# Kernel tuning notes

Measured on AMD Instinct MI355X. Metric: run time of the kernel, lower is better.

The kernel has to match this reference:

```python
import jax, jax.numpy as jnp
import numpy as np

B, S, HID, NH, HD, NL = 2, 4096, 1024, 16, 64, 128
N_ITER = 6


def setup_inputs() -> dict:
    key = jax.random.key(0)
    ks = jax.random.split(key, 9)
    s = 0.02
    D = NH * HD
    return {
        "X": jax.random.normal(ks[0], (B, S, HID), jnp.float32),
        "mask": jnp.ones((B, S), jnp.float32),
        "Wq": jax.random.normal(ks[1], (HID, D), jnp.float32) * s,
        "bq": jnp.zeros((D,), jnp.float32),
        "Wk": jax.random.normal(ks[2], (HID, D), jnp.float32) * s,
        "bk": jnp.zeros((D,), jnp.float32),
        "Wv": jax.random.normal(ks[3], (HID, D), jnp.float32) * s,
        "bv": jnp.zeros((D,), jnp.float32),
        "Wo": jax.random.normal(ks[4], (D, HID), jnp.float32) * s,
        "bo": jnp.zeros((HID,), jnp.float32),
    }


def iterative_inv(mat, n_iter=N_ITER):
    # Newton-Schulz style pseudo-inverse iteration (Nystromformer 'original' init)
    I = jnp.eye(mat.shape[-1], dtype=mat.dtype)
    K = mat
    V = K.swapaxes(-1, -2) / jnp.max(jnp.sum(K, axis=-2))
    for _ in range(n_iter):
        KV = K @ V
        V = 0.25 * V @ (13.0 * I - KV @ (15.0 * I - KV @ (7.0 * I - KV)))
    return V


def nystrom_core(Q, K, V, mask):
    # Q,K,V: [B,NH,S,HD], mask: [B,S]
    scale = 1.0 / np.sqrt(np.sqrt(HD))  # 1/d^(1/4) applied to both Q and K
    m = mask[:, None, :, None]
    Q = Q * m * scale
    K = K * m * scale
    seg = S // NL
    # landmarks: mean over contiguous segments -> [B,NH,NL,HD]
    Ql = Q.reshape(B, NH, NL, seg, HD).mean(axis=-2)
    Kl = K.reshape(B, NH, NL, seg, HD).mean(axis=-2)
    k1 = jax.nn.softmax(jnp.einsum('bhsd,bhld->bhsl', Q, Kl), axis=-1)   # [B,NH,S,NL]
    k2 = jax.nn.softmax(jnp.einsum('bhld,bhmd->bhlm', Ql, Kl), axis=-1)  # [B,NH,NL,NL]
    k3 = jax.nn.softmax(
        jnp.einsum('bhld,bhsd->bhls', Ql, K) - 1e9 * (1.0 - mask[:, None, None, :]),
        axis=-1)                                                          # [B,NH,NL,S]
    return k1 @ iterative_inv(k2) @ (k3 @ V)                              # [B,NH,S,HD]


def reference(X, mask, Wq, bq, Wk, bk, Wv, bv, Wo, bo):
    def split(Y):  # [B,S,NH*HD] -> [B,NH,S,HD]
        return Y.reshape(B, S, NH, HD).transpose(0, 2, 1, 3)
    Q = split(X @ Wq + bq)
    K = split(X @ Wk + bk)
    V = split(X @ Wv + bv)
    attn = nystrom_core(Q.astype(jnp.float32), K.astype(jnp.float32),
                        V.astype(jnp.float32), mask.astype(jnp.float32))
    out = attn.transpose(0, 2, 1, 3).reshape(B, S, NH * HD)
    return out @ Wo + bo
```

## Files before the change

### kernel.cpp

```cpp
#include <hip/hip_runtime.h>
#include <math.h>

constexpr int cB = 2, cS = 4096, cHID = 1024, cNH = 16, cHD = 64, cNL = 128, cSEG = 32, cD = 1024, cBH = 32;
constexpr float cSCALE = 0.35355339059327373f;

typedef _Float16 f16x8 __attribute__((ext_vector_type(8)));
typedef float f32x4 __attribute__((ext_vector_type(4)));

__device__ inline void gload_lds16(const void* g, void* l) {
    __builtin_amdgcn_global_load_lds(
        (const __attribute__((address_space(1))) void*)g,
        (__attribute__((address_space(3))) void*)l, 16, 0, 0);
}

__global__ __launch_bounds__(256) void wcast_t(
    const float* __restrict__ Wq, const float* __restrict__ Wk,
    const float* __restrict__ Wv, const float* __restrict__ Wo,
    _Float16* __restrict__ WqT, _Float16* __restrict__ WkT,
    _Float16* __restrict__ WvT, _Float16* __restrict__ WoT)
{
    __shared__ float tile[32][33];
    const int wsel = blockIdx.z;
    const float* W = (wsel == 0) ? Wq : (wsel == 1 ? Wk : (wsel == 2 ? Wv : Wo));
    _Float16* WT   = (wsel == 0) ? WqT : (wsel == 1 ? WkT : (wsel == 2 ? WvT : WoT));
    const int n0 = blockIdx.x * 32, k0 = blockIdx.y * 32;
    const int t = threadIdx.x;
    const int r = t >> 3, c = (t & 7) * 4;
    float4 v = *reinterpret_cast<const float4*>(W + (size_t)(k0 + r) * cD + n0 + c);
    tile[r][c] = v.x; tile[r][c + 1] = v.y; tile[r][c + 2] = v.z; tile[r][c + 3] = v.w;
    __syncthreads();
    union { _Float16 h[4]; ushort4 u; } p;
    p.h[0] = (_Float16)tile[c + 0][r]; p.h[1] = (_Float16)tile[c + 1][r];
    p.h[2] = (_Float16)tile[c + 2][r]; p.h[3] = (_Float16)tile[c + 3][r];
    *reinterpret_cast<ushort4*>(WT + (size_t)(n0 + r) * cHID + k0 + c) = p.u;
}

__global__ __launch_bounds__(256) void xm_kernel(
    const float* __restrict__ X, const float* __restrict__ mask,
    float* __restrict__ Xm, float* __restrict__ mbar, _Float16* __restrict__ Xh)
{
    const int bl = blockIdx.x;
    const int b = bl >> 7, l = bl & 127;
    const int c = threadIdx.x * 4;
    float4 a = {0.f, 0.f, 0.f, 0.f};
    float msum = 0.f;
    for (int j = 0; j < cSEG; ++j) {
        float m = mask[b * cS + l * cSEG + j];
        size_t roff = ((size_t)(b * cS + l * cSEG + j)) * cHID + c;
        float4 x = *reinterpret_cast<const float4*>(X + roff);
        union { _Float16 h[4]; ushort4 u; } p;
        p.h[0] = (_Float16)x.x; p.h[1] = (_Float16)x.y;
        p.h[2] = (_Float16)x.z; p.h[3] = (_Float16)x.w;
        *reinterpret_cast<ushort4*>(Xh + roff) = p.u;
        a.x += m * x.x; a.y += m * x.y; a.z += m * x.z; a.w += m * x.w;
        msum += m;
    }
    const float inv = 1.0f / cSEG;
    a.x *= inv; a.y *= inv; a.z *= inv; a.w *= inv;
    *reinterpret_cast<float4*>(Xm + (size_t)bl * cHID + c) = a;
    if (threadIdx.x == 0) mbar[bl] = msum * inv;
}

__global__ __launch_bounds__(256) void qkv_gemm_f16(
    const _Float16* __restrict__ Xh, const float* __restrict__ mask,
    const _Float16* __restrict__ WqT, const _Float16* __restrict__ WkT, const _Float16* __restrict__ WvT,
    const float* __restrict__ bq, const float* __restrict__ bk, const float* __restrict__ bv,
    _Float16* __restrict__ Qh, _Float16* __restrict__ Kh, _Float16* __restrict__ Vh)
{
    __shared__ __align__(16) _Float16 As[128 * 64];
    __shared__ __align__(16) _Float16 Bs[128 * 64];
    const int wsel = blockIdx.z;
    const _Float16* WT = (wsel == 0) ? WqT : (wsel == 1 ? WkT : WvT);
    const float* bias  = (wsel == 0) ? bq  : (wsel == 1 ? bk  : bv);
    _Float16* Y        = (wsel == 0) ? Qh  : (wsel == 1 ? Kh  : Vh);
    const int orig = blockIdx.x;
    const int xcd = orig & 7, idx = orig >> 3;
    const int n0 = (idx & 7) * 128;
    const int m0 = (xcd * 8 + (idx >> 3)) * 128;
    const int t = threadIdx.x;
    const int wave = t >> 6, lane = t & 63;
    const int wm = (wave >> 1) * 64, wn = (wave & 1) * 64;
    const int quad = lane >> 4, l15 = lane & 15;
    const int srow = wave * 8 + (lane >> 3);
    const int scol = ((lane & 7) ^ (lane >> 3)) * 8;

    f32x4 acc[4][4];
#pragma unroll
    for (int i = 0; i < 4; ++i)
#pragma unroll
        for (int j = 0; j < 4; ++j) acc[i][j] = (f32x4){0.f, 0.f, 0.f, 0.f};

    for (int k0 = 0; k0 < cHID; k0 += 64) {
        const _Float16* aSrc = Xh + (size_t)(m0 + srow) * cHID + k0 + scol;
// ... 180 lines not shown
#pragma unroll
    for (int u = 0; u < 16; ++u) {
        float4 a = q4[u], b = kl4[u];
        dot += a.x * b.x + a.y * b.y + a.z * b.z + a.w * b.w;
    }
    red[j] = dot; __syncthreads();
    for (int off = 64; off > 0; off >>= 1) { if (j < off) red[j] = fmaxf(red[j], red[j + off]); __syncthreads(); }
    float m = red[0]; __syncthreads();
    float e = expf(dot - m);
    red[j] = e; __syncthreads();
    for (int off = 64; off > 0; off >>= 1) { if (j < off) red[j] += red[j + off]; __syncthreads(); }
    k2[(bh * cNL + i) * cNL + j] = e / red[0];
}

__global__ __launch_bounds__(128) void colsum_max(const float* __restrict__ k2, int* __restrict__ cmax)
{
    __shared__ float red[128];
    int bh = blockIdx.x, j = threadIdx.x;
    float s = 0.f;
    for (int i = 0; i < cNL; ++i) s += k2[(bh * cNL + i) * cNL + j];
    red[j] = s; __syncthreads();
    for (int off = 64; off > 0; off >>= 1) { if (j < off) red[j] = fmaxf(red[j], red[j + off]); __syncthreads(); }
    if (j == 0) atomicMax(cmax, __float_as_int(red[0]));
}

__device__ inline void split2(float v, _Float16& h, _Float16& l) {
    h = (_Float16)v;
    l = (_Float16)(v - (float)h);
}
__device__ inline unsigned short f16bits(_Float16 h) { return __builtin_bit_cast(unsigned short, h); }

#define NYS_MFMA(a, b, c) __builtin_amdgcn_mfma_f32_16x16x32_f16((a), (b), (c), 0, 0, 0)

#define NYS_PRELOAD(PH, PL, LH, LL)                                                     \
    {                                                                                   \
        _Pragma("unroll")                                                               \
        for (int mt_ = 0; mt_ < 4; ++mt_) {                                             \
            const int rowL_ = wr * 64 + mt_ * 16 + l15;                                 \
            _Pragma("unroll")                                                           \
            for (int k0_ = 0; k0_ < 4; ++k0_) {                                         \
                LH[mt_][k0_] = *reinterpret_cast<const f16x8*>(&PH[rowL_ * 136 + k0_ * 32 + quad * 8]); \
                LL[mt_][k0_] = *reinterpret_cast<const f16x8*>(&PL[rowL_ * 136 + k0_ * 32 + quad * 8]); \
            }                                                                           \
        }                                                                               \
    }

#define NYS_PRODUCT(PH, PL, LH, LL)                                                     \
    {                                                                                   \
        _Pragma("unroll")                                                               \
        for (int mt_ = 0; mt_ < 4; ++mt_)                                               \
            _Pragma("unroll")                                                           \
            for (int nt_ = 0; nt_ < 2; ++nt_) acc[mt_][nt_] = (f32x4){0.f, 0.f, 0.f, 0.f}; \
        _Pragma("unroll")                                                               \
        for (int nt_ = 0; nt_ < 2; ++nt_) {                                             \
            _Pragma("unroll")                                                           \
            for (int k0_ = 0; k0_ < 4; ++k0_) {                                         \
                const int boff_ = (wcb + nt_ * 16) * 136 + k0_ * 32 + quad * 8;         \
                f16x8 bh_ = *reinterpret_cast<const f16x8*>(&PH[boff_]);                \
                f16x8 bl_ = *reinterpret_cast<const f16x8*>(&PL[boff_]);                \
                _Pragma("unroll")                                                       \
                for (int mt_ = 0; mt_ < 4; ++mt_) {                                     \
                    acc[mt_][nt_] = NYS_MFMA(LH[mt_][k0_], bh_, acc[mt_][nt_]);         \
                    acc[mt_][nt_] = NYS_MFMA(LL[mt_][k0_], bh_, acc[mt_][nt_]);         \
                    acc[mt_][nt_] = NYS_MFMA(LH[mt_][k0_], bl_, acc[mt_][nt_]);         \
                }                                                                       \
            }                                                                           \
        }                                                                               \
    }

__global__ __launch_bounds__(512, 2) void nys_fused(
    const float* __restrict__ k2, const int* __restrict__ cmax,
    float* __restrict__ Mg0, float* __restrict__ Mg1)
{
    __shared__ __align__(16) _Float16 Ahi_s[128 * 136];
    __shared__ __align__(16) _Float16 Alo_s[128 * 136];
    __shared__ __align__(16) _Float16 Whi_s[128 * 136];
    __shared__ __align__(16) _Float16 Wlo_s[128 * 136];
    const int bh = blockIdx.x;
    const int t = threadIdx.x;
    const int wave = t >> 6, lane = t & 63;
    const int wr = wave >> 2, wc = wave & 3;
    const int quad = lane >> 4, l15 = lane & 15;
    const int wcb = wc * 32 + l15;
    const float* Kg = k2 + (size_t)bh * 16384;
    float* Mg0b = Mg0 + (size_t)bh * 16384;
    float* Mg1b = Mg1 + (size_t)bh * 16384;
    const float sc = sqrtf(1.0f / __int_as_float(*cmax));

    {
        const int row = t >> 2, c0 = (t & 3) * 32;
        const float* src = Kg + row * 128 + c0;
        _Float16* dh = &Whi_s[row * 136 + c0];
        _Float16* dl = &Wlo_s[row * 136 + c0];
#pragma unroll
        for (int u = 0; u < 32; u += 4) {
            float4 v = *reinterpret_cast<const float4*>(src + u);
            ushort4 ph, pl; _Float16 h, l;
            split2(v.x * sc, h, l); ph.x = f16bits(h); pl.x = f16bits(l);
            split2(v.y * sc, h, l); ph.y = f16bits(h); pl.y = f16bits(l);
            split2(v.z * sc, h, l); ph.z = f16bits(h); pl.z = f16bits(l);
            split2(v.w * sc, h, l); ph.w = f16bits(h); pl.w = f16bits(l);
            *reinterpret_cast<ushort4*>(dh + u) = ph;
            *reinterpret_cast<ushort4*>(dl + u) = pl;
        }
    }
    __syncthreads();

    f32x4 acc[4][2];
    f16x8 Fh[4][4], Fl[4][4];

    NYS_PRELOAD(Whi_s, Wlo_s, Fh, Fl);
    NYS_PRODUCT(Whi_s, Wlo_s, Fh, Fl);
#pragma unroll
    for (int mt = 0; mt < 4; ++mt)
#pragma unroll
        for (int nt = 0; nt < 2; ++nt) {
            const int col = wcb + nt * 16;
            const int rb  = wr * 64 + mt * 16 + quad * 4;
            ushort4 ph, pl;
#pragma unroll
            for (int r = 0; r < 4; ++r) {
                _Float16 h, l; split2(acc[mt][nt][r], h, l);
                ((unsigned short*)&ph)[r] = f16bits(h);
                ((unsigned short*)&pl)[r] = f16bits(l);
            }
            *reinterpret_cast<ushort4*>(&Ahi_s[col * 136 + rb]) = ph;
            *reinterpret_cast<ushort4*>(&Alo_s[col * 136 + rb]) = pl;
        }
    __syncthreads();

    for (int it = 0; it < 6; ++it) {
        NYS_PRELOAD(Ahi_s, Alo_s, Fh, Fl);
        NYS_PRODUCT(Ahi_s, Alo_s, Fh, Fl);
#pragma unroll
        for (int mt = 0; mt < 4; ++mt)
#pragma unroll
            for (int nt = 0; nt < 2; ++nt) {
                const int col = wcb + nt * 16;
                const int rb  = wr * 64 + mt * 16 + quad * 4;
                ushort4 ah = *reinterpret_cast<const ushort4*>(&Ahi_s[col * 136 + rb]);
                ushort4 al = *reinterpret_cast<const ushort4*>(&Alo_s[col * 136 + rb]);
                ushort4 ph, pl;
#pragma unroll
                for (int r = 0; r < 4; ++r) {
                    float av = (float)__builtin_bit_cast(_Float16, ((unsigned short*)&ah)[r])
                             + (float)__builtin_bit_cast(_Float16, ((unsigned short*)&al)[r]);
                    float v = ((rb + r) == col ? 15.0f : 0.0f) - 7.0f * av + acc[mt][nt][r];
                    _Float16 h, l; split2(v, h, l);
                    ((unsigned short*)&ph)[r] = f16bits(h);
                    ((unsigned short*)&pl)[r] = f16bits(l);
                }
                *reinterpret_cast<ushort4*>(&Whi_s[col * 136 + rb]) = ph;
                *reinterpret_cast<ushort4*>(&Wlo_s[col * 136 + rb]) = pl;
            }
        __syncthreads();
        NYS_PRODUCT(Whi_s, Wlo_s, Fh, Fl);
        __syncthreads();
#pragma unroll
        for (int mt = 0; mt < 4; ++mt)
#pragma unroll
            for (int nt = 0; nt < 2; ++nt) {
                const int col = wcb + nt * 16;
                const int rb  = wr * 64 + mt * 16 + quad * 4;
                ushort4 ph, pl; float4 mv;
#pragma unroll
                for (int r = 0; r < 4; ++r) {
                    float v = ((rb + r) == col ? 13.0f : 0.0f) - acc[mt][nt][r];
                    _Float16 h, l; split2(v, h, l);
                    ((unsigned short*)&ph)[r] = f16bits(h);
                    ((unsigned short*)&pl)[r] = f16bits(l);
                    ((float*)&mv)[r] = 0.25f * v;
                }
                *reinterpret_cast<ushort4*>(&Whi_s[col * 136 + rb]) = ph;
                *reinterpret_cast<ushort4*>(&Wlo_s[col * 136 + rb]) = pl;
                if (it == 0)
                    *reinterpret_cast<float4*>(&Mg0b[col * 128 + rb]) = mv;
            }
        __syncthreads();
        NYS_PRODUCT(Whi_s, Wlo_s, Fh, Fl);
#pragma unroll
        for (int mt = 0; mt < 4; ++mt)
#pragma unroll
            for (int nt = 0; nt < 2; ++nt) {
                const int col = wcb + nt * 16;
                const int rb  = wr * 64 + mt * 16 + quad * 4;
                ushort4 ph, pl;
#pragma unroll
                for (int r = 0; r < 4; ++r) {
                    _Float16 h, l; split2(0.25f * acc[mt][nt][r], h, l);
                    ((unsigned short*)&ph)[r] = f16bits(h);
                    ((unsigned short*)&pl)[r] = f16bits(l);
                }
                *reinterpret_cast<ushort4*>(&Ahi_s[col * 136 + rb]) = ph;
                *reinterpret_cast<ushort4*>(&Alo_s[col * 136 + rb]) = pl;
            }
        if (it >= 1) {
            const float* Mr = (it & 1) ? Mg0b : Mg1b;
            float*       Mw = (it & 1) ? Mg1b : Mg0b;
#pragma unroll
            for (int mt = 0; mt < 4; ++mt)
#pragma unroll
                for (int nt = 0; nt < 2; ++nt) acc[mt][nt] = (f32x4){0.f, 0.f, 0.f, 0.f};
#pragma unroll
            for (int k0 = 0; k0 < 4; ++k0) {
                f16x8 Mh[4], Ml[4];
#pragma unroll
                for (int mt = 0; mt < 4; ++mt) {
                    const int rowL = wr * 64 + mt * 16 + l15;
                    const float* src = Mr + rowL * 128 + k0 * 32 + quad * 8;
                    float4 v0 = *reinterpret_cast<const float4*>(src);
                    float4 v1 = *reinterpret_cast<const float4*>(src + 4);
                    union { f16x8 v; _Float16 e[8]; } hh, ll;
                    split2(v0.x, hh.e[0], ll.e[0]); split2(v0.y, hh.e[1], ll.e[1]);
                    split2(v0.z, hh.e[2], ll.e[2]); split2(v0.w, hh.e[3], ll.e[3]);
                    split2(v1.x, hh.e[4], ll.e[4]); split2(v1.y, hh.e[5], ll.e[5]);
                    split2(v1.z, hh.e[6], ll.e[6]); split2(v1.w, hh.e[7], ll.e[7]);
                    Mh[mt] = hh.v; Ml[mt] = ll.v;
                }
#pragma unroll
                for (int nt = 0; nt < 2; ++nt) {
                    const int boff = (wcb + nt * 16) * 136 + k0 * 32 + quad * 8;
                    f16x8 bh_ = *reinterpret_cast<const f16x8*>(&Whi_s[boff]);
                    f16x8 bl_ = *reinterpret_cast<const f16x8*>(&Wlo_s[boff]);
#pragma unroll
                    for (int mt = 0; mt < 4; ++mt) {
                        acc[mt][nt] = NYS_MFMA(Mh[mt], bh_, acc[mt][nt]);
                        acc[mt][nt] = NYS_MFMA(Ml[mt], bh_, acc[mt][nt]);
                        acc[mt][nt] = NYS_MFMA(Mh[mt], bl_, acc[mt][nt]);
                    }
                }
            }
#pragma unroll
            for (int mt = 0; mt < 4; ++mt)
#pragma unroll
                for (int nt = 0; nt < 2; ++nt) {
                    const int col = wcb + nt * 16;
                    const int rb  = wr * 64 + mt * 16 + quad * 4;
                    float4 mv;
#pragma unroll
                    for (int r = 0; r < 4; ++r) ((float*)&mv)[r] = 0.25f * acc[mt][nt][r];
                    *reinterpret_cast<float4*>(&Mw[col * 128 + rb]) = mv;
                }
        }
        __syncthreads();
    }
}

__global__ __launch_bounds__(256) void vtrans(const _Float16* __restrict__ Vh, _Float16* __restrict__ VTh)
{
    __shared__ ushort T[64][72];
    const int s0 = blockIdx.x * 64, bh = blockIdx.y;
    const int t = threadIdx.x;
    const _Float16* vb = Vh + ((size_t)bh * cS + s0) * cHD;
#pragma unroll
    for (int i = 0; i < 2; ++i) {
        int idx = t + i * 256;
        int row = idx >> 3, c8 = idx & 7;
        f16x8 v = *reinterpret_cast<const f16x8*>(vb + (size_t)row * cHD + c8 * 8);
#pragma unroll
        for (int j = 0; j < 8; ++j) T[row][c8 * 8 + j] = ((ushort*)&v)[j];
    }
    __syncthreads();
    _Float16* vt = VTh + (size_t)bh * cHD * cS;
#pragma unroll
    for (int i = 0; i < 2; ++i) {
        int idx = t + i * 256;
        int d = idx >> 3, s8 = idx & 7;
        f16x8 o;
#pragma unroll
        for (int j = 0; j < 8; ++j) ((ushort*)&o)[j] = T[s8 * 8 + j][d];
        *reinterpret_cast<f16x8*>(vt + (size_t)d * cS + s0 + s8 * 8) = o;
    }
}

__global__ __launch_bounds__(256) void k3v_mfma(
    const _Float16* __restrict__ Qlh, const _Float16* __restrict__ Kh,
    const _Float16* __restrict__ VTh, const float* __restrict__ mask,
    float* __restrict__ Opart, float* __restrict__ mpart, float* __restrict__ spart)
{
    __shared__ __align__(16) _Float16 Ps[128 * 72];
    __shared__ float msk[256];
    const int z = blockIdx.x, bh = blockIdx.y;
    const int b = bh >> 4;
    const int sbase = z * 256;
    const int t = threadIdx.x;
    const int wave = t >> 6, lane = t & 63;
    const int quad = lane >> 4, l15 = lane & 15;

    msk[t] = mask[b * cS + sbase + t];

    f16x8 aq[2][2];
    const _Float16* qlg = Qlh + (size_t)bh * cNL * cHD;
#pragma unroll
    for (int mt = 0; mt < 2; ++mt)
#pragma unroll
        for (int k0 = 0; k0 < 2; ++k0)
            aq[mt][k0] = *reinterpret_cast<const f16x8*>(
                qlg + (size_t)(wave * 32 + mt * 16 + l15) * cHD + k0 * 32 + quad * 8);

    float mrun[2][4], srun[2][4];
    f32x4 accO[2][4];
#pragma unroll
    for (int mt = 0; mt < 2; ++mt)
#pragma unroll
        for (int r = 0; r < 4; ++r) { mrun[mt][r] = -1e30f; srun[mt][r] = 0.f; }
#pragma unroll
    for (int mt = 0; mt < 2; ++mt)
#pragma unroll
        for (int dt = 0; dt < 4; ++dt) accO[mt][dt] = (f32x4){0.f, 0.f, 0.f, 0.f};

    __syncthreads();

    const _Float16* kg = Kh + (size_t)bh * cS * cHD;
    const _Float16* vg = VTh + (size_t)bh * cHD * cS;

    for (int step = 0; step < 4; ++step) {
        const int st = sbase + step * 64;
        f32x4 accS[2][4];
#pragma unroll
        for (int mt = 0; mt < 2; ++mt)
#pragma unroll
            for (int nt = 0; nt < 4; ++nt) accS[mt][nt] = (f32x4){0.f, 0.f, 0.f, 0.f};
#pragma unroll
        for (int k0 = 0; k0 < 2; ++k0)
#pragma unroll
            for (int nt = 0; nt < 4; ++nt) {
                f16x8 bk = *reinterpret_cast<const f16x8*>(
                    kg + (size_t)(st + nt * 16 + l15) * cHD + k0 * 32 + quad * 8);
#pragma unroll
                for (int mt = 0; mt < 2; ++mt)
                    accS[mt][nt] = __builtin_amdgcn_mfma_f32_16x16x32_f16(aq[mt][k0], bk, accS[mt][nt], 0, 0, 0);
            }
#pragma unroll
        for (int nt = 0; nt < 4; ++nt) {
            float pen = 1e9f * (1.0f - msk[step * 64 + nt * 16 + l15]);
#pragma unroll
            for (int mt = 0; mt < 2; ++mt)
#pragma unroll
                for (int r = 0; r < 4; ++r) accS[mt][nt][r] -= pen;
        }
#pragma unroll
        for (int mt = 0; mt < 2; ++mt) {
#pragma unroll
            for (int r = 0; r < 4; ++r) {
                float tmax = fmaxf(fmaxf(accS[mt][0][r], accS[mt][1][r]),
                                   fmaxf(accS[mt][2][r], accS[mt][3][r]));
#pragma unroll
                for (int w = 1; w < 16; w <<= 1) tmax = fmaxf(tmax, __shfl_xor(tmax, w, 16));
                float mnew = fmaxf(mrun[mt][r], tmax);
                float alpha = __expf(mrun[mt][r] - mnew);
                float ts = 0.f;
#pragma unroll
                for (int nt = 0; nt < 4; ++nt) {
                    float e = __expf(accS[mt][nt][r] - mnew);
                    accS[mt][nt][r] = e; ts += e;
                }
#pragma unroll
                for (int w = 1; w < 16; w <<= 1) ts += __shfl_xor(ts, w, 16);
                srun[mt][r] = srun[mt][r] * alpha + ts;
                mrun[mt][r] = mnew;
#pragma unroll
                for (int dt = 0; dt < 4; ++dt) accO[mt][dt][r] *= alpha;
            }
        }
#pragma unroll
        for (int mt = 0; mt < 2; ++mt)
#pragma unroll
            for (int nt = 0; nt < 4; ++nt)
#pragma unroll
                for (int r = 0; r < 4; ++r)
                    Ps[(wave * 32 + mt * 16 + quad * 4 + r) * 72 + nt * 16 + l15] =
                        (_Float16)accS[mt][nt][r];
#pragma unroll
        for (int k0 = 0; k0 < 2; ++k0) {
            f16x8 ap[2];
#pragma unroll
            for (int mt = 0; mt < 2; ++mt)
                ap[mt] = *reinterpret_cast<const f16x8*>(
                    &Ps[(wave * 32 + mt * 16 + l15) * 72 + k0 * 32 + quad * 8]);
#pragma unroll
            for (int dt = 0; dt < 4; ++dt) {
                f16x8 bv = *reinterpret_cast<const f16x8*>(
                    vg + (size_t)(dt * 16 + l15) * cS + st + k0 * 32 + quad * 8);
#pragma unroll
                for (int mt = 0; mt < 2; ++mt)
                    accO[mt][dt] = __builtin_amdgcn_mfma_f32_16x16x32_f16(ap[mt], bv, accO[mt][dt], 0, 0, 0);
            }
        }
    }
    const int rowbase = bh * cNL + wave * 32;
#pragma unroll
    for (int mt = 0; mt < 2; ++mt)
#pragma unroll
        for (int dt = 0; dt < 4; ++dt)
#pragma unroll
            for (int r = 0; r < 4; ++r)
                Opart[(size_t)(z * 4096 + rowbase + mt * 16 + quad * 4 + r) * cHD + dt * 16 + l15] =
                    accO[mt][dt][r];
    if (l15 == 0) {
#pragma unroll
        for (int mt = 0; mt < 2; ++mt)
#pragma unroll
            for (int r = 0; r < 4; ++r) {
                int prow = z * 4096 + rowbase + mt * 16 + quad * 4 + r;
                mpart[prow] = mrun[mt][r];
                spart[prow] = srun[mt][r];
            }
    }
}

__global__ __launch_bounds__(256) void k3v_reduce(
    const float* __restrict__ Opart, const float* __restrict__ mpart,
    const float* __restrict__ spart, float* __restrict__ CV)
{
    const int t = threadIdx.x;
    const int row = blockIdx.x * 4 + (t >> 6);
    const int d = t & 63;
    float mstar = -1e30f;
#pragma unroll
    for (int z = 0; z < 16; ++z) mstar = fmaxf(mstar, mpart[z * 4096 + row]);
    float ssum = 0.f, acc = 0.f;
#pragma unroll
    for (int z = 0; z < 16; ++z) {
        float w = __expf(mpart[z * 4096 + row] - mstar);
        ssum += w * spart[z * 4096 + row];
        acc  += w * Opart[(size_t)(z * 4096 + row) * cHD + d];
    }
    CV[(size_t)row * cHD + d] = acc / ssum;
}

__global__ __launch_bounds__(256) void w2_matmul(
    const float* __restrict__ k2, const float* __restrict__ M6,
    const int* __restrict__ cmax, const float* __restrict__ CV,
    _Float16* __restrict__ W2T)
{
    __shared__ __align__(16) float CVs[128][68];
    __shared__ __align__(16) float Us[128][68];
    const int bh = blockIdx.x, t = threadIdx.x;
    const float invc = 1.0f / __int_as_float(*cmax);
    for (int k = 0; k < 32; ++k) { int idx = t + k * 256; CVs[idx >> 6][idx & 63] = CV[(size_t)bh * 8192 + idx]; }
// ... 129 lines not shown
{
    const float* X    = (const float*)d_in[0];
    const float* mask = (const float*)d_in[1];
    const float* Wq   = (const float*)d_in[2];
    const float* bq   = (const float*)d_in[3];
    const float* Wk   = (const float*)d_in[4];
    const float* bk   = (const float*)d_in[5];
    const float* Wv   = (const float*)d_in[6];
    const float* bv   = (const float*)d_in[7];
    const float* Wo   = (const float*)d_in[8];
    const float* bo   = (const float*)d_in[9];
    float* out = (float*)d_out;

    float* ws = (float*)d_ws;
    size_t off = 0;
    const size_t szQKV = (size_t)cBH * cS * cHD;
    const size_t szL   = (size_t)cBH * cNL * cHD;
    const size_t szM   = (size_t)cBH * cNL * cNL;
    float* Qr   = ws + off; off += szQKV;
    float* Kr   = ws + off; off += szQKV;
    float* Vr   = ws + off; off += szQKV;
    _Float16* Xh  = (_Float16*)(ws + off); off += szQKV / 2;
    _Float16* WqT = (_Float16*)(ws + off); off += 524288;
    _Float16* WkT = (_Float16*)(ws + off); off += 524288;
    _Float16* WvT = (_Float16*)(ws + off); off += 524288;
    _Float16* WoT = (_Float16*)(ws + off); off += 524288;
    float* Xm   = ws + off; off += (size_t)cB * cNL * cHID;
    float* mbar = ws + off; off += 256;
    float* Ql  = ws + off; off += szL;
    float* Kl  = ws + off; off += szL;
    float* k2  = ws + off; off += szM;
    float* Mg0 = ws + off; off += szM;
    float* Mg1 = ws + off; off += szM;
    float* Zb  = ws + off; off += szM;
    float* T2b = ws + off; off += szM;
    float* T3b = ws + off; off += szM;
    float* CV  = ws + off; off += szL;
    _Float16* Qlh  = (_Float16*)(ws + off); off += szL / 2;
    _Float16* Klh  = (_Float16*)(ws + off); off += szL / 2;
    _Float16* W2Th = (_Float16*)(ws + off); off += szL / 2;
    int*   cmax = (int*)(ws + off); off += 16;
    float* mpart = ws + off; off += 65536;
    float* spart = ws + off; off += 65536;

    _Float16* Qh   = (_Float16*)Qr;
    float*    Opart = Qr + szQKV / 2;
    _Float16* Kh   = (_Float16*)Kr;
    _Float16* ctxh = (_Float16*)(Kr + szQKV / 2);
    _Float16* Vh   = (_Float16*)Vr;
    _Float16* VTh  = (_Float16*)(Vr + szQKV / 2);

    (void)Zb; (void)T2b; (void)T3b;

    hipMemsetAsync(cmax, 0, sizeof(int), stream);

    wcast_t<<<dim3(32, 32, 4), 256, 0, stream>>>(Wq, Wk, Wv, Wo, WqT, WkT, WvT, WoT);
    xm_kernel<<<cB * cNL, 256, 0, stream>>>(X, mask, Xm, mbar, Xh);

    qkv_gemm_f16<<<dim3(512, 1, 3), 256, 0, stream>>>(
        Xh, mask, WqT, WkT, WvT, bq, bk, bv, Qh, Kh, Vh);
    vtrans<<<dim3(cS / 64, cBH), 256, 0, stream>>>(Vh, VTh);
    lgemm<<<dim3(cD / 64, (cB * cNL) / 64, 2), 256, 0, stream>>>(Xm, mbar, Wq, bq, Wk, bk, Ql, Kl, Qlh, Klh);

    k2_softmax<<<cBH * cNL, 128, 0, stream>>>(Ql, Kl, k2);
    colsum_max<<<cBH, 128, 0, stream>>>(k2, cmax);

    nys_fused<<<cBH, 512, 0, stream>>>(k2, cmax, Mg0, Mg1);

    k3v_mfma<<<dim3(16, cBH), 256, 0, stream>>>(Qlh, Kh, VTh, mask, Opart, mpart, spart);
    k3v_reduce<<<1024, 256, 0, stream>>>(Opart, mpart, spart, CV);
    w2_matmul<<<cBH, 256, 0, stream>>>(k2, Mg1, cmax, CV, W2Th);
    k1_mfma<<<dim3(cS / 64, cBH), 256, 0, stream>>>(Qh, Klh, W2Th, ctxh);
    out_gemm_f16<<<dim3(512), 256, 0, stream>>>(ctxh, WoT, bo, out);
}
```

Baseline: 474.2 us.

## Fuse Nystrom inverse and k3V into one launch and halve inverse-kernel LDS

The Newton-Schulz inverse kernel (32 blocks) and the k3·V flash-style kernel (16×32 blocks) are merged into one launch keyed on blockIdx. The independent k3V work now runs alongside the long serial inverse iterations instead of after them. To fit two blocks per CU with the k3V blocks, the inverse path keeps only the W operand in LDS and reads the A matrix from a global fp32 scratch buffer, splitting it to hi/lo fp16 on the fly. This adds global traffic and conversion work inside the iteration. The xm_kernel is also reshaped to use 4× more blocks of 64 threads for more parallelism.

```diff
diff --git a/kernel.cpp b/kernel.cpp
--- a/kernel.cpp
+++ b/kernel.cpp
@@ -35,13 +35,14 @@
     *reinterpret_cast<ushort4*>(WT + (size_t)(n0 + r) * cHID + k0 + c) = p.u;
 }
 
-__global__ __launch_bounds__(256) void xm_kernel(
+__global__ __launch_bounds__(64) void xm_kernel(
     const float* __restrict__ X, const float* __restrict__ mask,
     float* __restrict__ Xm, float* __restrict__ mbar, _Float16* __restrict__ Xh)
 {
     const int bl = blockIdx.x;
+    const int q  = blockIdx.y;
     const int b = bl >> 7, l = bl & 127;
-    const int c = threadIdx.x * 4;
+    const int c = q * 256 + threadIdx.x * 4;
     float4 a = {0.f, 0.f, 0.f, 0.f};
     float msum = 0.f;
     for (int j = 0; j < cSEG; ++j) {
@@ -58,7 +59,7 @@
     const float inv = 1.0f / cSEG;
     a.x *= inv; a.y *= inv; a.z *= inv; a.w *= inv;
     *reinterpret_cast<float4*>(Xm + (size_t)bl * cHID + c) = a;
-    if (threadIdx.x == 0) mbar[bl] = msum * inv;
+    if (q == 0 && threadIdx.x == 0) mbar[bl] = msum * inv;
 }
 
 __global__ __launch_bounds__(256) void qkv_gemm_f16(
@@ -305,7 +306,7 @@
 
 #define NYS_MFMA(a, b, c) __builtin_amdgcn_mfma_f32_16x16x32_f16((a), (b), (c), 0, 0, 0)
 
-#define NYS_PRELOAD(PH, PL, LH, LL)                                                     \
+#define NYS_PRELOAD_LDS(PH, PL, LH, LL)                                                 \
     {                                                                                   \
         _Pragma("unroll")                                                               \
         for (int mt_ = 0; mt_ < 4; ++mt_) {                                             \
@@ -318,7 +319,27 @@
         }                                                                               \
     }
 
-#define NYS_PRODUCT(PH, PL, LH, LL)                                                     \
+#define NYS_PRELOAD_G(GP, LH, LL)                                                       \
+    {                                                                                   \
+        _Pragma("unroll")                                                               \
+        for (int mt_ = 0; mt_ < 4; ++mt_) {                                             \
+            const int rowL_ = wr * 64 + mt_ * 16 + l15;                                 \
+            _Pragma("unroll")                                                           \
+            for (int k0_ = 0; k0_ < 4; ++k0_) {                                         \
+                const float* s_ = GP + rowL_ * 128 + k0_ * 32 + quad * 8;               \
+                float4 v0_ = *reinterpret_cast<const float4*>(s_);                      \
+                float4 v1_ = *reinterpret_cast<const float4*>(s_ + 4);                  \
+                union { f16x8 v; _Float16 e[8]; } hh_, ll_;                             \
+                split2(v0_.x, hh_.e[0], ll_.e[0]); split2(v0_.y, hh_.e[1], ll_.e[1]);   \
+                split2(v0_.z, hh_.e[2], ll_.e[2]); split2(v0_.w, hh_.e[3], ll_.e[3]);   \
+                split2(v1_.x, hh_.e[4], ll_.e[4]); split2(v1_.y, hh_.e[5], ll_.e[5]);   \
+                split2(v1_.z, hh_.e[6], ll_.e[6]); split2(v1_.w, hh_.e[7], ll_.e[7]);   \
+                LH[mt_][k0_] = hh_.v; LL[mt_][k0_] = ll_.v;                             \
+            }                                                                           \
+        }                                                                               \
+    }
+
+#define NYS_PRODUCT_LDS(PH, PL, LH, LL)                                                 \
     {                                                                                   \
         _Pragma("unroll")                                                               \
         for (int mt_ = 0; mt_ < 4; ++mt_)                                               \
@@ -341,168 +362,141 @@
         }                                                                               \
     }
 
-__global__ __launch_bounds__(512, 2) void nys_fused(
+#define NYS_PRODUCT_G(GP, LH, LL)                                                       \
+    {                                                                                   \
+        _Pragma("unroll")                                                               \
+        for (int mt_ = 0; mt_ < 4; ++mt_)                                               \
+            _Pragma("unroll")                                                           \
+            for (int nt_ = 0; nt_ < 2; ++nt_) acc[mt_][nt_] = (f32x4){0.f, 0.f, 0.f, 0.f}; \
+        _Pragma("unroll")                                                               \
+        for (int nt_ = 0; nt_ < 2; ++nt_) {                                             \
+            _Pragma("unroll")                                                           \
+            for (int k0_ = 0; k0_ < 4; ++k0_) {                                         \
+                const float* s_ = GP + (wcb + nt_ * 16) * 128 + k0_ * 32 + quad * 8;    \
+                float4 v0_ = *reinterpret_cast<const float4*>(s_);                      \
+                float4 v1_ = *reinterpret_cast<const float4*>(s_ + 4);                  \
+                union { f16x8 v; _Float16 e[8]; } bh_, bl_;                             \
+                split2(v0_.x, bh_.e[0], bl_.e[0]); split2(v0_.y, bh_.e[1], bl_.e[1]);   \
+                split2(v0_.z, bh_.e[2], bl_.e[2]); split2(v0_.w, bh_.e[3], bl_.e[3]);   \
+                split2(v1_.x, bh_.e[4], bl_.e[4]); split2(v1_.y, bh_.e[5], bl_.e[5]);   \
+                split2(v1_.z, bh_.e[6], bl_.e[6]); split2(v1_.w, bh_.e[7], bl_.e[7]);   \
+                _Pragma("unroll")                                                       \
+                for (int mt_ = 0; mt_ < 4; ++mt_) {                                     \
+                    acc[mt_][nt_] = NYS_MFMA(LH[mt_][k0_], bh_.v, acc[mt_][nt_]);       \
+                    acc[mt_][nt_] = NYS_MFMA(LL[mt_][k0_], bh_.v, acc[mt_][nt_]);       \
+                    acc[mt_][nt_] = NYS_MFMA(LH[mt_][k0_], bl_.v, acc[mt_][nt_]);       \
+                }                                                                       \
+            }                                                                           \
+        }                                                                               \
+    }
+
+__global__ __launch_bounds__(512, 2) void nys_k3v(
     const float* __restrict__ k2, const int* __restrict__ cmax,
-    float* __restrict__ Mg0, float* __restrict__ Mg1)
-{
-    __shared__ __align__(16) _Float16 Ahi_s[128 * 136];
-    __shared__ __align__(16) _Float16 Alo_s[128 * 136];
-    __shared__ __align__(16) _Float16 Whi_s[128 * 136];
-    __shared__ __align__(16) _Float16 Wlo_s[128 * 136];
-    const int bh = blockIdx.x;
-    const int t = threadIdx.x;
-    const int wave = t >> 6, lane = t & 63;
-    const int wr = wave >> 2, wc = wave & 3;
-    const int quad = lane >> 4, l15 = lane & 15;
-    const int wcb = wc * 32 + l15;
-    const float* Kg = k2 + (size_t)bh * 16384;
-    float* Mg0b = Mg0 + (size_t)bh * 16384;
-    float* Mg1b = Mg1 + (size_t)bh * 16384;
-    const float sc = sqrtf(1.0f / __int_as_float(*cmax));
-
-    {
-        const int row = t >> 2, c0 = (t & 3) * 32;
-        const float* src = Kg + row * 128 + c0;
-        _Float16* dh = &Whi_s[row * 136 + c0];
-        _Float16* dl = &Wlo_s[row * 136 + c0];
-#pragma unroll
-        for (int u = 0; u < 32; u += 4) {
-            float4 v = *reinterpret_cast<const float4*>(src + u);
-            ushort4 ph, pl; _Float16 h, l;
-            split2(v.x * sc, h, l); ph.x = f16bits(h); pl.x = f16bits(l);
-            split2(v.y * sc, h, l); ph.y = f16bits(h); pl.y = f16bits(l);
-            split2(v.z * sc, h, l); ph.z = f16bits(h); pl.z = f16bits(l);
-            split2(v.w * sc, h, l); ph.w = f16bits(h); pl.w = f16bits(l);
-            *reinterpret_cast<ushort4*>(dh + u) = ph;
-            *reinterpret_cast<ushort4*>(dl + u) = pl;
-        }
-    }
-    __syncthreads();
-
-    f32x4 acc[4][2];
-    f16x8 Fh[4][4], Fl[4][4];
-
-    NYS_PRELOAD(Whi_s, Wlo_s, Fh, Fl);
-    NYS_PRODUCT(Whi_s, Wlo_s, Fh, Fl);
-#pragma unroll
-    for (int mt = 0; mt < 4; ++mt)
-#pragma unroll
-        for (int nt = 0; nt < 2; ++nt) {
-            const int col = wcb + nt * 16;
-            const int rb  = wr * 64 + mt * 16 + quad * 4;
-            ushort4 ph, pl;
-#pragma unroll
-            for (int r = 0; r < 4; ++r) {
-                _Float16 h, l; split2(acc[mt][nt][r], h, l);
-                ((unsigned short*)&ph)[r] = f16bits(h);
-                ((unsigned short*)&pl)[r] = f16bits(l);
+    float* __restrict__ Ag_all, float* __restrict__ Mg0, float* __restrict__ Mg1,
+    const _Float16* __restrict__ Qlh, const _Float16* __restrict__ Kh,
+    const _Float16* __restrict__ VTh, const float* __restrict__ mask,
+    float* __restrict__ Opart, float* __restrict__ mpart, float* __restrict__ spart)
+{
+    __shared__ __align__(16) _Float16 SMEM[2 * 128 * 136];
+
+    if (blockIdx.x < 32) {
+        _Float16* Wh = SMEM;
+        _Float16* Wl = SMEM + 128 * 136;
+        const int bh = blockIdx.x;
+        const int t = threadIdx.x;
+        const int wave = t >> 6, lane = t & 63;
+        const int wr = wave >> 2, wc = wave & 3;
+        const int quad = lane >> 4, l15 = lane & 15;
+        const int wcb = wc * 32 + l15;
+        const float* Kg = k2 + (size_t)bh * 16384;
+        float* Ag   = Ag_all + (size_t)bh * 16384;
+        float* Mg0b = Mg0 + (size_t)bh * 16384;
+        float* Mg1b = Mg1 + (size_t)bh * 16384;
+        const float sc = sqrtf(1.0f / __int_as_float(*cmax));
+
+        {
+            const int row = t >> 2, c0 = (t & 3) * 32;
+            const float* src = Kg + row * 128 + c0;
+            _Float16* dh = &Wh[row * 136 + c0];
+            _Float16* dl = &Wl[row * 136 + c0];
+#pragma unroll
+            for (int u = 0; u < 32; u += 4) {
+                float4 v = *reinterpret_cast<const float4*>(src + u);
+                ushort4 ph, pl; _Float16 h, l;
+                split2(v.x * sc, h, l); ph.x = f16bits(h); pl.x = f16bits(l);
+                split2(v.y * sc, h, l); ph.y = f16bits(h); pl.y = f16bits(l);
+                split2(v.z * sc, h, l); ph.z = f16bits(h); pl.z = f16bits(l);
+                split2(v.w * sc, h, l); ph.w = f16bits(h); pl.w = f16bits(l);
+                *reinterpret_cast<ushort4*>(dh + u) = ph;
+                *reinterpret_cast<ushort4*>(dl + u) = pl;
             }
-            *reinterpret_cast<ushort4*>(&Ahi_s[col * 136 + rb]) = ph;
-            *reinterpret_cast<ushort4*>(&Alo_s[col * 136 + rb]) = pl;
-        }
-    __syncthreads();
-
-    for (int it = 0; it < 6; ++it) {
-        NYS_PRELOAD(Ahi_s, Alo_s, Fh, Fl);
-        NYS_PRODUCT(Ahi_s, Alo_s, Fh, Fl);
+        }
+        __syncthreads();
+
+        f32x4 acc[4][2];
+        f16x8 Fh[4][4], Fl[4][4];
+
+        NYS_PRELOAD_LDS(Wh, Wl, Fh, Fl);
+        NYS_PRODUCT_LDS(Wh, Wl, Fh, Fl);
 #pragma unroll
         for (int mt = 0; mt < 4; ++mt)
 #pragma unroll
             for (int nt = 0; nt < 2; ++nt) {
                 const int col = wcb + nt * 16;
                 const int rb  = wr * 64 + mt * 16 + quad * 4;
-                ushort4 ah = *reinterpret_cast<const ushort4*>(&Ahi_s[col * 136 + rb]);
-                ushort4 al = *reinterpret_cast<const ushort4*>(&Alo_s[col * 136 + rb]);
-                ushort4 ph, pl;
-#pragma unroll
-                for (int r = 0; r < 4; ++r) {
-                    float av = (float)__builtin_bit_cast(_Float16, ((unsigned short*)&ah)[r])
-                             + (float)__builtin_bit_cast(_Float16, ((unsigned short*)&al)[r]);
-                    float v = ((rb + r) == col ? 15.0f : 0.0f) - 7.0f * av + acc[mt][nt][r];
-                    _Float16 h, l; split2(v, h, l);
-                    ((unsigned short*)&ph)[r] = f16bits(h);
-                    ((unsigned short*)&pl)[r] = f16bits(l);
-                }
-                *reinterpret_cast<ushort4*>(&Whi_s[col * 136 + rb]) = ph;
-                *reinterpret_cast<ushort4*>(&Wlo_s[col * 136 + rb]) = pl;
+                float4 mv;
+#pragma unroll
+                for (int r = 0; r < 4; ++r) ((float*)&mv)[r] = acc[mt][nt][r];
+                *reinterpret_cast<float4*>(&Ag[col * 128 + rb]) = mv;
             }
         __syncthreads();
-        NYS_PRODUCT(Whi_s, Wlo_s, Fh, Fl);
-        __syncthreads();
-#pragma unroll
-        for (int mt = 0; mt < 4; ++mt)
-#pragma unroll
-            for (int nt = 0; nt < 2; ++nt) {
-                const int col = wcb + nt * 16;
-                const int rb  = wr * 64 + mt * 16 + quad * 4;
-                ushort4 ph, pl; float4 mv;
-#pragma unroll
-                for (int r = 0; r < 4; ++r) {
-                    float v = ((rb + r) == col ? 13.0f : 0.0f) - acc[mt][nt][r];
-                    _Float16 h, l; split2(v, h, l);
-                    ((unsigned short*)&ph)[r] = f16bits(h);
-                    ((unsigned short*)&pl)[r] = f16bits(l);
-                    ((float*)&mv)[r] = 0.25f * v;
+
+        for (int it = 0; it < 6; ++it) {
+            NYS_PRELOAD_G(Ag, Fh, Fl);
+            NYS_PRODUCT_G(Ag, Fh, Fl);
+#pragma unroll
+            for (int mt = 0; mt < 4; ++mt)
+#pragma unroll
+                for (int nt = 0; nt < 2; ++nt) {
+                    const int col = wcb + nt * 16;
+                    const int rb  = wr * 64 + mt * 16 + quad * 4;
+                    float4 av = *reinterpret_cast<const float4*>(&Ag[col * 128 + rb]);
+                    ushort4 ph, pl;
+#pragma unroll
+                    for (int r = 0; r < 4; ++r) {
+                        float v = ((rb + r) == col ? 15.0f : 0.0f) - 7.0f * ((float*)&av)[r] + acc[mt][nt][r];
+                        _Float16 h, l; split2(v, h, l);
+                        ((unsigned short*)&ph)[r] = f16bits(h);
+                        ((unsigned short*)&pl)[r] = f16bits(l);
+                    }
+                    *reinterpret_cast<ushort4*>(&Wh[col * 136 + rb]) = ph;
+                    *reinterpret_cast<ushort4*>(&Wl[col * 136 + rb]) = pl;
                 }
-                *reinterpret_cast<ushort4*>(&Whi_s[col * 136 + rb]) = ph;
-                *reinterpret_cast<ushort4*>(&Wlo_s[col * 136 + rb]) = pl;
-                if (it == 0)
-                    *reinterpret_cast<float4*>(&Mg0b[col * 128 + rb]) = mv;
-            }
-        __syncthreads();
-        NYS_PRODUCT(Whi_s, Wlo_s, Fh, Fl);
-#pragma unroll
-        for (int mt = 0; mt < 4; ++mt)
-#pragma unroll
-            for (int nt = 0; nt < 2; ++nt) {
-                const int col = wcb + nt * 16;
-                const int rb  = wr * 64 + mt * 16 + quad * 4;
-                ushort4 ph, pl;
-#pragma unroll
-                for (int r = 0; r < 4; ++r) {
-                    _Float16 h, l; split2(0.25f * acc[mt][nt][r], h, l);
-                    ((unsigned short*)&ph)[r] = f16bits(h);
-                    ((unsigned short*)&pl)[r] = f16bits(l);
+            __syncthreads();
+            NYS_PRODUCT_LDS(Wh, Wl, Fh, Fl);
+            __syncthreads();
+#pragma unroll
+            for (int mt = 0; mt < 4; ++mt)
+#pragma unroll
+                for (int nt = 0; nt < 2; ++nt) {
+                    const int col = wcb + nt * 16;
+                    const int rb  = wr * 64 + mt * 16 + quad * 4;
+                    ushort4 ph, pl; float4 mv;
+#pragma unroll
+                    for (int r = 0; r < 4; ++r) {
+                        float v = ((rb + r) == col ? 13.0f : 0.0f) - acc[mt][nt][r];
+                        _Float16 h, l; split2(v, h, l);
+                        ((unsigned short*)&ph)[r] = f16bits(h);
+                        ((unsigned short*)&pl)[r] = f16bits(l);
+                        ((float*)&mv)[r] = 0.25f * v;
+                    }
+                    *reinterpret_cast<ushort4*>(&Wh[col * 136 + rb]) = ph;
+                    *reinterpret_cast<ushort4*>(&Wl[col * 136 + rb]) = pl;
+                    if (it == 0)
+                        *reinterpret_cast<float4*>(&Mg0b[col * 128 + rb]) = mv;
                 }
-                *reinterpret_cast<ushort4*>(&Ahi_s[col * 136 + rb]) = ph;
-                *reinterpret_cast<ushort4*>(&Alo_s[col * 136 + rb]) = pl;
-            }
-        if (it >= 1) {
-            const float* Mr = (it & 1) ? Mg0b : Mg1b;
-            float*       Mw = (it & 1) ? Mg1b : Mg0b;
-#pragma unroll
-            for (int mt = 0; mt < 4; ++mt)
-#pragma unroll
-                for (int nt = 0; nt < 2; ++nt) acc[mt][nt] = (f32x4){0.f, 0.f, 0.f, 0.f};
-#pragma unroll
-            for (int k0 = 0; k0 < 4; ++k0) {
-                f16x8 Mh[4], Ml[4];
-#pragma unroll
-                for (int mt = 0; mt < 4; ++mt) {
-                    const int rowL = wr * 64 + mt * 16 + l15;
-                    const float* src = Mr + rowL * 128 + k0 * 32 + quad * 8;
-                    float4 v0 = *reinterpret_cast<const float4*>(src);
-                    float4 v1 = *reinterpret_cast<const float4*>(src + 4);
-                    union { f16x8 v; _Float16 e[8]; } hh, ll;
-                    split2(v0.x, hh.e[0], ll.e[0]); split2(v0.y, hh.e[1], ll.e[1]);
-                    split2(v0.z, hh.e[2], ll.e[2]); split2(v0.w, hh.e[3], ll.e[3]);
-                    split2(v1.x, hh.e[4], ll.e[4]); split2(v1.y, hh.e[5], ll.e[5]);
-                    split2(v1.z, hh.e[6], ll.e[6]); split2(v1.w, hh.e[7], ll.e[7]);
-                    Mh[mt] = hh.v; Ml[mt] = ll.v;
-                }
-#pragma unroll
-                for (int nt = 0; nt < 2; ++nt) {
-                    const int boff = (wcb + nt * 16) * 136 + k0 * 32 + quad * 8;
-                    f16x8 bh_ = *reinterpret_cast<const f16x8*>(&Whi_s[boff]);
-                    f16x8 bl_ = *reinterpret_cast<const f16x8*>(&Wlo_s[boff]);
-#pragma unroll
-                    for (int mt = 0; mt < 4; ++mt) {
-                        acc[mt][nt] = NYS_MFMA(Mh[mt], bh_, acc[mt][nt]);
-                        acc[mt][nt] = NYS_MFMA(Ml[mt], bh_, acc[mt][nt]);
-                        acc[mt][nt] = NYS_MFMA(Mh[mt], bl_, acc[mt][nt]);
-                    }
-                }
-            }
+            __syncthreads();
+            NYS_PRODUCT_LDS(Wh, Wl, Fh, Fl);
 #pragma unroll
             for (int mt = 0; mt < 4; ++mt)
 #pragma unroll
@@ -512,10 +506,185 @@
                     float4 mv;
 #pragma unroll
                     for (int r = 0; r < 4; ++r) ((float*)&mv)[r] = 0.25f * acc[mt][nt][r];
-                    *reinterpret_cast<float4*>(&Mw[col * 128 + rb]) = mv;
+                    *reinterpret_cast<float4*>(&Ag[col * 128 + rb]) = mv;
                 }
-        }
-        __syncthreads();
+            if (it >= 1) {
+                const float* Mr = (it & 1) ? Mg0b : Mg1b;
+                float*       Mw = (it & 1) ? Mg1b : Mg0b;
+#pragma unroll
+                for (int mt = 0; mt < 4; ++mt)
+#pragma unroll
+                    for (int nt = 0; nt < 2; ++nt) acc[mt][nt] = (f32x4){0.f, 0.f, 0.f, 0.f};
+#pragma unroll
+                for (int k0 = 0; k0 < 4; ++k0) {
+                    f16x8 Mh[4], Ml[4];
+#pragma unroll
+                    for (int mt = 0; mt < 4; ++mt) {
+                        const int rowL = wr * 64 + mt * 16 + l15;
+                        const float* src = Mr + rowL * 128 + k0 * 32 + quad * 8;
+                        float4 v0 = *reinterpret_cast<const float4*>(src);
+                        float4 v1 = *reinterpret_cast<const float4*>(src + 4);
+                        union { f16x8 v; _Float16 e[8]; } hh, ll;
+                        split2(v0.x, hh.e[0], ll.e[0]); split2(v0.y, hh.e[1], ll.e[1]);
+                        split2(v0.z, hh.e[2], ll.e[2]); split2(v0.w, hh.e[3], ll.e[3]);
+                        split2(v1.x, hh.e[4], ll.e[4]); split2(v1.y, hh.e[5], ll.e[5]);
+                        split2(v1.z, hh.e[6], ll.e[6]); split2(v1.w, hh.e[7], ll.e[7]);
+                        Mh[mt] = hh.v; Ml[mt] = ll.v;
+                    }
+#pragma unroll
+                    for (int nt = 0; nt < 2; ++nt) {
+                        const int boff = (wcb + nt * 16) * 136 + k0 * 32 + quad * 8;
+                        f16x8 bh_ = *reinterpret_cast<const f16x8*>(&Wh[boff]);
+                        f16x8 bl_ = *reinterpret_cast<const f16x8*>(&Wl[boff]);
+#pragma unroll
+                        for (int mt = 0; mt < 4; ++mt) {
+                            acc[mt][nt] = NYS_MFMA(Mh[mt], bh_, acc[mt][nt]);
+                            acc[mt][nt] = NYS_MFMA(Ml[mt], bh_, acc[mt][nt]);
+                            acc[mt][nt] = NYS_MFMA(Mh[mt], bl_, acc[mt][nt]);
+                        }
+                    }
+                }
+#pragma unroll
+                for (int mt = 0; mt < 4; ++mt)
+#pragma unroll
+                    for (int nt = 0; nt < 2; ++nt) {
+                        const int col = wcb + nt * 16;
+                        const int rb  = wr * 64 + mt * 16 + quad * 4;
+                        float4 mv;
+#pragma unroll
+                        for (int r = 0; r < 4; ++r) ((float*)&mv)[r] = 0.25f * acc[mt][nt][r];
+                        *reinterpret_cast<float4*>(&Mw[col * 128 + rb]) = mv;
+                    }
+            }
+            __syncthreads();
+        }
+    } else {
+        if (threadIdx.x >= 256) return;
+        _Float16* Ps = SMEM;
+        const int id = blockIdx.x - 32;
+        const int z = id & 15, bh = id >> 4;
+        const int b = bh >> 4;
+        const int sbase = z * 256;
+        const int t = threadIdx.x;
+        const int wave = t >> 6, lane = t & 63;
+        const int quad = lane >> 4, l15 = lane & 15;
+
+        f16x8 aq[2][2];
+        const _Float16* qlg = Qlh + (size_t)bh * cNL * cHD;
+#pragma unroll
+        for (int mt = 0; mt < 2; ++mt)
+#pragma unroll
+            for (int k0 = 0; k0 < 2; ++k0)
+                aq[mt][k0] = *reinterpret_cast<const f16x8*>(
+                    qlg + (size_t)(wave * 32 + mt * 16 + l15) * cHD + k0 * 32 + quad * 8);
+
+        float mrun[2][4], srun[2][4];
+        f32x4 accO[2][4];
+#pragma unroll
+        for (int mt = 0; mt < 2; ++mt)
+#pragma unroll
+            for (int r = 0; r < 4; ++r) { mrun[mt][r] = -1e30f; srun[mt][r] = 0.f; }
+#pragma unroll
+        for (int mt = 0; mt < 2; ++mt)
+#pragma unroll
+            for (int dt = 0; dt < 4; ++dt) accO[mt][dt] = (f32x4){0.f, 0.f, 0.f, 0.f};
+
+        const _Float16* kg = Kh + (size_t)bh * cS * cHD;
+        const _Float16* vg = VTh + (size_t)bh * cHD * cS;
+
+        for (int step = 0; step < 4; ++step) {
+            const int st = sbase + step * 64;
+            f32x4 accS[2][4];
+#pragma unroll
+            for (int mt = 0; mt < 2; ++mt)
+#pragma unroll
+                for (int nt = 0; nt < 4; ++nt) accS[mt][nt] = (f32x4){0.f, 0.f, 0.f, 0.f};
+#pragma unroll
+            for (int k0 = 0; k0 < 2; ++k0)
+#pragma unroll
+                for (int nt = 0; nt < 4; ++nt) {
+                    f16x8 bk = *reinterpret_cast<const f16x8*>(
+                        kg + (size_t)(st + nt * 16 + l15) * cHD + k0 * 32 + quad * 8);
+#pragma unroll
+                    for (int mt = 0; mt < 2; ++mt)
+                        accS[mt][nt] = __builtin_amdgcn_mfma_f32_16x16x32_f16(aq[mt][k0], bk, accS[mt][nt], 0, 0, 0);
+                }
+#pragma unroll
+            for (int nt = 0; nt < 4; ++nt) {
+                float pen = 1e9f * (1.0f - mask[b * cS + st + nt * 16 + l15]);
+#pragma unroll
+                for (int mt = 0; mt < 2; ++mt)
+#pragma unroll
+                    for (int r = 0; r < 4; ++r) accS[mt][nt][r] -= pen;
+            }
+#pragma unroll
+            for (int mt = 0; mt < 2; ++mt) {
+#pragma unroll
+                for (int r = 0; r < 4; ++r) {
+                    float tmax = fmaxf(fmaxf(accS[mt][0][r], accS[mt][1][r]),
+                                       fmaxf(accS[mt][2][r], accS[mt][3][r]));
+#pragma unroll
+                    for (int w = 1; w < 16; w <<= 1) tmax = fmaxf(tmax, __shfl_xor(tmax, w, 16));
+                    float mnew = fmaxf(mrun[mt][r], tmax);
+                    float alpha = __expf(mrun[mt][r] - mnew);
+                    float ts = 0.f;
+#pragma unroll
+                    for (int nt = 0; nt < 4; ++nt) {
+                        float e = __expf(accS[mt][nt][r] - mnew);
+                        accS[mt][nt][r] = e; ts += e;
+                    }
+#pragma unroll
+                    for (int w = 1; w < 16; w <<= 1) ts += __shfl_xor(ts, w, 16);
+                    srun[mt][r] = srun[mt][r] * alpha + ts;
+                    mrun[mt][r] = mnew;
+#pragma unroll
+                    for (int dt = 0; dt < 4; ++dt) accO[mt][dt][r] *= alpha;
+                }
+            }
+#pragma unroll
+            for (int mt = 0; mt < 2; ++mt)
+#pragma unroll
+                for (int nt = 0; nt < 4; ++nt)
+#pragma unroll
+                    for (int r = 0; r < 4; ++r)
+                        Ps[(wave * 32 + mt * 16 + quad * 4 + r) * 72 + nt * 16 + l15] =
+                            (_Float16)accS[mt][nt][r];
+#pragma unroll
+            for (int k0 = 0; k0 < 2; ++k0) {
+                f16x8 ap[2];
+#pragma unroll
+                for (int mt = 0; mt < 2; ++mt)
+                    ap[mt] = *reinterpret_cast<const f16x8*>(
+                        &Ps[(wave * 32 + mt * 16 + l15) * 72 + k0 * 32 + quad * 8]);
+#pragma unroll
+                for (int dt = 0; dt < 4; ++dt) {
+                    f16x8 bv = *reinterpret_cast<const f16x8*>(
+                        vg + (size_t)(dt * 16 + l15) * cS + st + k0 * 32 + quad * 8);
+#pragma unroll
+                    for (int mt = 0; mt < 2; ++mt)
+                        accO[mt][dt] = __builtin_amdgcn_mfma_f32_16x16x32_f16(ap[mt], bv, accO[mt][dt], 0, 0, 0);
+                }
+            }
+        }
+        const int rowbase = bh * cNL + wave * 32;
+#pragma unroll
+        for (int mt = 0; mt < 2; ++mt)
+#pragma unroll
+            for (int dt = 0; dt < 4; ++dt)
+#pragma unroll
+                for (int r = 0; r < 4; ++r)
+                    Opart[(size_t)(z * 4096 + rowbase + mt * 16 + quad * 4 + r) * cHD + dt * 16 + l15] =
+                        accO[mt][dt][r];
+        if (l15 == 0) {
+#pragma unroll
+            for (int mt = 0; mt < 2; ++mt)
+#pragma unroll
+                for (int r = 0; r < 4; ++r) {
+                    int prow = z * 4096 + rowbase + mt * 16 + quad * 4 + r;
+                    mpart[prow] = mrun[mt][r];
+                    spart[prow] = srun[mt][r];
+                }
+        }
     }
 }
 
@@ -543,142 +712,6 @@
 #pragma unroll
         for (int j = 0; j < 8; ++j) ((ushort*)&o)[j] = T[s8 * 8 + j][d];
         *reinterpret_cast<f16x8*>(vt + (size_t)d * cS + s0 + s8 * 8) = o;
-    }
-}
-
-__global__ __launch_bounds__(256) void k3v_mfma(
-    const _Float16* __restrict__ Qlh, const _Float16* __restrict__ Kh,
-    const _Float16* __restrict__ VTh, const float* __restrict__ mask,
-    float* __restrict__ Opart, float* __restrict__ mpart, float* __restrict__ spart)
-{
-    __shared__ __align__(16) _Float16 Ps[128 * 72];
-    __shared__ float msk[256];
-    const int z = blockIdx.x, bh = blockIdx.y;
-    const int b = bh >> 4;
-    const int sbase = z * 256;
-    const int t = threadIdx.x;
-    const int wave = t >> 6, lane = t & 63;
-    const int quad = lane >> 4, l15 = lane & 15;
-
-    msk[t] = mask[b * cS + sbase + t];
-
-    f16x8 aq[2][2];
-    const _Float16* qlg = Qlh + (size_t)bh * cNL * cHD;
-#pragma unroll
-    for (int mt = 0; mt < 2; ++mt)
-#pragma unroll
-        for (int k0 = 0; k0 < 2; ++k0)
-            aq[mt][k0] = *reinterpret_cast<const f16x8*>(
-                qlg + (size_t)(wave * 32 + mt * 16 + l15) * cHD + k0 * 32 + quad * 8);
-
-    float mrun[2][4], srun[2][4];
-    f32x4 accO[2][4];
-#pragma unroll
-    for (int mt = 0; mt < 2; ++mt)
-#pragma unroll
-        for (int r = 0; r < 4; ++r) { mrun[mt][r] = -1e30f; srun[mt][r] = 0.f; }
-#pragma unroll
-    for (int mt = 0; mt < 2; ++mt)
-#pragma unroll
-        for (int dt = 0; dt < 4; ++dt) accO[mt][dt] = (f32x4){0.f, 0.f, 0.f, 0.f};
-
-    __syncthreads();
-
-    const _Float16* kg = Kh + (size_t)bh * cS * cHD;
-    const _Float16* vg = VTh + (size_t)bh * cHD * cS;
-
-    for (int step = 0; step < 4; ++step) {
-        const int st = sbase + step * 64;
-        f32x4 accS[2][4];
-#pragma unroll
-        for (int mt = 0; mt < 2; ++mt)
-#pragma unroll
-            for (int nt = 0; nt < 4; ++nt) accS[mt][nt] = (f32x4){0.f, 0.f, 0.f, 0.f};
-#pragma unroll
-        for (int k0 = 0; k0 < 2; ++k0)
-#pragma unroll
-            for (int nt = 0; nt < 4; ++nt) {
-                f16x8 bk = *reinterpret_cast<const f16x8*>(
-                    kg + (size_t)(st + nt * 16 + l15) * cHD + k0 * 32 + quad * 8);
-#pragma unroll
-                for (int mt = 0; mt < 2; ++mt)
-                    accS[mt][nt] = __builtin_amdgcn_mfma_f32_16x16x32_f16(aq[mt][k0], bk, accS[mt][nt], 0, 0, 0);
-            }
-#pragma unroll
-        for (int nt = 0; nt < 4; ++nt) {
-            float pen = 1e9f * (1.0f - msk[step * 64 + nt * 16 + l15]);
-#pragma unroll
-            for (int mt = 0; mt < 2; ++mt)
-#pragma unroll
-                for (int r = 0; r < 4; ++r) accS[mt][nt][r] -= pen;
-        }
-#pragma unroll
-        for (int mt = 0; mt < 2; ++mt) {
-#pragma unroll
-            for (int r = 0; r < 4; ++r) {
-                float tmax = fmaxf(fmaxf(accS[mt][0][r], accS[mt][1][r]),
-                                   fmaxf(accS[mt][2][r], accS[mt][3][r]));
-#pragma unroll
-                for (int w = 1; w < 16; w <<= 1) tmax = fmaxf(tmax, __shfl_xor(tmax, w, 16));
-                float mnew = fmaxf(mrun[mt][r], tmax);
-                float alpha = __expf(mrun[mt][r] - mnew);
-                float ts = 0.f;
-#pragma unroll
-                for (int nt = 0; nt < 4; ++nt) {
-                    float e = __expf(accS[mt][nt][r] - mnew);
-                    accS[mt][nt][r] = e; ts += e;
-                }
-#pragma unroll
-                for (int w = 1; w < 16; w <<= 1) ts += __shfl_xor(ts, w, 16);
-                srun[mt][r] = srun[mt][r] * alpha + ts;
-                mrun[mt][r] = mnew;
-#pragma unroll
-                for (int dt = 0; dt < 4; ++dt) accO[mt][dt][r] *= alpha;
-            }
-        }
-#pragma unroll
-        for (int mt = 0; mt < 2; ++mt)
-#pragma unroll
-            for (int nt = 0; nt < 4; ++nt)
-#pragma unroll
-                for (int r = 0; r < 4; ++r)
-                    Ps[(wave * 32 + mt * 16 + quad * 4 + r) * 72 + nt * 16 + l15] =
-                        (_Float16)accS[mt][nt][r];
-#pragma unroll
-        for (int k0 = 0; k0 < 2; ++k0) {
-            f16x8 ap[2];
-#pragma unroll
-            for (int mt = 0; mt < 2; ++mt)
-                ap[mt] = *reinterpret_cast<const f16x8*>(
-                    &Ps[(wave * 32 + mt * 16 + l15) * 72 + k0 * 32 + quad * 8]);
-#pragma unroll
-            for (int dt = 0; dt < 4; ++dt) {
-                f16x8 bv = *reinterpret_cast<const f16x8*>(
-                    vg + (size_t)(dt * 16 + l15) * cS + st + k0 * 32 + quad * 8);
-#pragma unroll
-                for (int mt = 0; mt < 2; ++mt)
-                    accO[mt][dt] = __builtin_amdgcn_mfma_f32_16x16x32_f16(ap[mt], bv, accO[mt][dt], 0, 0, 0);
-            }
-        }
-    }
-    const int rowbase = bh * cNL + wave * 32;
-#pragma unroll
-    for (int mt = 0; mt < 2; ++mt)
-#pragma unroll
-        for (int dt = 0; dt < 4; ++dt)
-#pragma unroll
-            for (int r = 0; r < 4; ++r)
-                Opart[(size_t)(z * 4096 + rowbase + mt * 16 + quad * 4 + r) * cHD + dt * 16 + l15] =
-                    accO[mt][dt][r];
-    if (l15 == 0) {
-#pragma unroll
-        for (int mt = 0; mt < 2; ++mt)
-#pragma unroll
-            for (int r = 0; r < 4; ++r) {
-                int prow = z * 4096 + rowbase + mt * 16 + quad * 4 + r;
-                mpart[prow] = mrun[mt][r];
-                spart[prow] = srun[mt][r];
-            }
     }
 }
 
@@ -874,7 +907,7 @@
     float* k2  = ws + off; off += szM;
     float* Mg0 = ws + off; off += szM;
     float* Mg1 = ws + off; off += szM;
-    float* Zb  = ws + off; off += szM;
+    float* Agb = ws + off; off += szM;
     float* T2b = ws + off; off += szM;
     float* T3b = ws + off; off += szM;
     float* CV  = ws + off; off += szL;
@@ -892,12 +925,12 @@
     _Float16* Vh   = (_Float16*)Vr;
     _Float16* VTh  = (_Float16*)(Vr + szQKV / 2);
 
-    (void)Zb; (void)T2b; (void)T3b;
+    (void)T2b; (void)T3b;
 
     hipMemsetAsync(cmax, 0, sizeof(int), stream);
 
     wcast_t<<<dim3(32, 32, 4), 256, 0, stream>>>(Wq, Wk, Wv, Wo, WqT, WkT, WvT, WoT);
-    xm_kernel<<<cB * cNL, 256, 0, stream>>>(X, mask, Xm, mbar, Xh);
+    xm_kernel<<<dim3(cB * cNL, 4), 64, 0, stream>>>(X, mask, Xm, mbar, Xh);
 
     qkv_gemm_f16<<<dim3(512, 1, 3), 256, 0, stream>>>(
         Xh, mask, WqT, WkT, WvT, bq, bk, bv, Qh, Kh, Vh);
@@ -907,9 +940,9 @@
     k2_softmax<<<cBH * cNL, 128, 0, stream>>>(Ql, Kl, k2);
     colsum_max<<<cBH, 128, 0, stream>>>(k2, cmax);
 
-    nys_fused<<<cBH, 512, 0, stream>>>(k2, cmax, Mg0, Mg1);
-
-    k3v_mfma<<<dim3(16, cBH), 256, 0, stream>>>(Qlh, Kh, VTh, mask, Opart, mpart, spart);
+    nys_k3v<<<dim3(32 + 16 * cBH), 512, 0, stream>>>(
+        k2, cmax, Agb, Mg0, Mg1, Qlh, Kh, VTh, mask, Opart, mpart, spart);
+
     k3v_reduce<<<1024, 256, 0, stream>>>(Opart, mpart, spart, CV);
     w2_matmul<<<cBH, 256, 0, stream>>>(k2, Mg1, cmax, CV, W2Th);
     k1_mfma<<<dim3(cS / 64, cBH), 256, 0, stream>>>(Qh, Klh, W2Th, ctxh);
```

After: 519.6 us. 9.6% more time.
